# Kernel tuning notes

Measured on AMD Instinct MI355X. Metric: run time of the kernel, lower is better.

## Reference

```python
import jax, jax.numpy as jnp
import numpy as np

# Static config (matches init_kwargs)
T_Q, H_Q, W_Q = 8, 16, 16
T_K, H_K, W_K = 8, 16, 16
HEADS, QDIM = 8, 64


def _rel_dist(q_len, k_len):
    q_ratio = round(max(k_len / q_len, 1.0))
    k_ratio = round(max(q_len / k_len, 1.0))
    d = jnp.arange(q_len)[:, None] * q_ratio - jnp.arange(k_len)[None, :] * k_ratio
    return d + (k_len - 1) * k_ratio  # [q_len, k_len] int indices


def setup_inputs() -> dict:
    key = jax.random.key(0)
    k1, k2, k3, k4, k5 = jax.random.split(key, 5)
    B = 2
    q_tok = T_Q * H_Q * W_Q
    k_tok = T_K * H_K * W_K
    return {
        "query": jax.random.normal(k1, (B, HEADS, q_tok, QDIM), dtype=jnp.float32),
        "scores": jax.random.normal(k2, (B, HEADS, q_tok, k_tok), dtype=jnp.float32),
        "height_emb": jax.random.normal(k3, (2 * (max(H_Q, H_K) - 1) + 1, QDIM), dtype=jnp.float32),
        "width_emb": jax.random.normal(k4, (2 * (max(W_Q, W_K) - 1) + 1, QDIM), dtype=jnp.float32),
        "time_emb": jax.random.normal(k5, (2 * (max(T_Q, T_K) - 1) + 1, QDIM), dtype=jnp.float32),
    }


def reference(query, scores, height_emb, width_emb, time_emb):
    B = query.shape[0]
    # Relative-distance index tables (static)
    dist_h = _rel_dist(H_Q, H_K)  # [H_Q, H_K]
    dist_w = _rel_dist(W_Q, W_K)  # [W_Q, W_K]
    dist_t = _rel_dist(T_Q, T_K)  # [T_Q, T_K]
    Rh = height_emb[dist_h]  # [H_Q, H_K, C]
    Rw = width_emb[dist_w]   # [W_Q, W_K, C]
    Rt = time_emb[dist_t]    # [T_Q, T_K, C]
    q = query.reshape(B, HEADS, T_Q, H_Q, W_Q, QDIM)
    rel_h = jnp.einsum('bNthwc,hkc->bNthwk', q, Rh)  # k = key height
    rel_w = jnp.einsum('bNthwc,wkc->bNthwk', q, Rw)  # k = key width
    rel_t = jnp.einsum('bNthwc,tkc->bNthwk', q, Rt)  # k = key time
    s = scores.reshape(B, HEADS, T_Q, H_Q, W_Q, T_K, H_K, W_K)
    s = (s
         + rel_h[:, :, :, :, :, None, :, None]
         + rel_w[:, :, :, :, :, None, None, :]
         + rel_t[:, :, :, :, :, :, None, None])
    return s.reshape(B, HEADS, T_Q * H_Q * W_Q, T_K * H_K * W_K)
```

## Files before the change

kernel.cpp:

```cpp
#include <hip/hip_runtime.h>

#define T_Q 8
#define H_Q 16
#define W_Q 16
#define HEADS 8
#define QDIM 64
#define QTOK (T_Q * H_Q * W_Q)
#define KTOK 2048

__global__ __launch_bounds__(256)
void relpos_fused_kernel(const float* __restrict__ query,
                         const float* __restrict__ scores,
                         const float* __restrict__ hemb,
                         const float* __restrict__ wemb,
                         const float* __restrict__ temb,
                         float* __restrict__ out)
{
    const int row  = blockIdx.x;
    const int qtok = row & (QTOK - 1);
    const int t = (qtok >> 8) & 7;
    const int h = (qtok >> 4) & 15;
    const int w = qtok & 15;
    const int tid = threadIdx.x;

    __shared__ float q_s[QDIM];
    __shared__ float rel[40];

    if (tid < QDIM) q_s[tid] = query[(size_t)row * QDIM + tid];
    __syncthreads();

    if (tid < 40) {
        const float* emb;
        if (tid < 16) {
            emb = hemb + (size_t)(h - tid + 15) * QDIM;
        } else if (tid < 32) {
            emb = wemb + (size_t)(w - (tid - 16) + 15) * QDIM;
        } else {
            emb = temb + (size_t)(t - (tid - 32) + 7) * QDIM;
        }
        float acc = 0.f;
        #pragma unroll
        for (int c = 0; c < QDIM; c += 4) {
            float4 e = *reinterpret_cast<const float4*>(emb + c);
            acc += q_s[c]   * e.x;
            acc += q_s[c+1] * e.y;
            acc += q_s[c+2] * e.z;
            acc += q_s[c+3] * e.w;
        }
        rel[tid] = acc;
    }
    __syncthreads();

    const size_t base = (size_t)row * KTOK;
    #pragma unroll
    for (int it = 0; it < 2; ++it) {
        const int k4 = (it * 256 + tid) * 4;
        const int tk = k4 >> 8;
        const int hk = (k4 >> 4) & 15;
        const int wk = k4 & 15;
        const float add = rel[32 + tk] + rel[hk];
        float4 s = *reinterpret_cast<const float4*>(scores + base + k4);
        float4 o;
        o.x = s.x + add + rel[16 + wk + 0];
        o.y = s.y + add + rel[16 + wk + 1];
        o.z = s.z + add + rel[16 + wk + 2];
        o.w = s.w + add + rel[16 + wk + 3];
        *reinterpret_cast<float4*>(out + base + k4) = o;
    }
}

extern "C" void kernel_launch(void* const* d_in, const int* in_sizes, int n_in,
                              void* d_out, int out_size, void* d_ws, size_t ws_size,
                              hipStream_t stream) {
    const float* query  = (const float*)d_in[0];
    const float* scores = (const float*)d_in[1];
    const float* hemb   = (const float*)d_in[2];
    const float* wemb   = (const float*)d_in[3];
    const float* temb   = (const float*)d_in[4];
    float* out = (float*)d_out;

    const int B = in_sizes[0] / (HEADS * QTOK * QDIM);
    const int rows = B * HEADS * QTOK;

    relpos_fused_kernel<<<rows, 256, 0, stream>>>(query, scores, hemb, wemb, temb, out);
}
```

Measured before the change: 104.5 us.

## Map one wavefront per row and stream scores with nontemporal loads/stores

Each 256-thread block now handles four rows, one per 64-lane wavefront, so the grid shrinks by four. Every wave computes its own 40 relative-position dot products. Each lane keeps a fixed key h/w position across eight iterations, so the per-element adds are hoisted into registers. Scores and outputs use nontemporal loads and stores to skip cache pollution on this streaming, memory-bound workload, and the embedding dot product now reads q from shared memory as float4.

Result: faster. 100.5 us (-3.9%).

```diff
diff --git a/kernel.cpp b/kernel.cpp
--- a/kernel.cpp
+++ b/kernel.cpp
@@ -8,6 +8,8 @@
 #define QTOK (T_Q * H_Q * W_Q)
 #define KTOK 2048
 
+typedef float f32x4 __attribute__((ext_vector_type(4)));
+
 __global__ __launch_bounds__(256)
 void relpos_fused_kernel(const float* __restrict__ query,
                          const float* __restrict__ scores,
@@ -16,56 +18,63 @@
                          const float* __restrict__ temb,
                          float* __restrict__ out)
 {
-    const int row  = blockIdx.x;
+    const int tid  = threadIdx.x;
+    const int wid  = tid >> 6;
+    const int lane = tid & 63;
+    const int row  = blockIdx.x * 4 + wid;
     const int qtok = row & (QTOK - 1);
     const int t = (qtok >> 8) & 7;
     const int h = (qtok >> 4) & 15;
     const int w = qtok & 15;
-    const int tid = threadIdx.x;
 
-    __shared__ float q_s[QDIM];
-    __shared__ float rel[40];
+    __shared__ float q_s[4][QDIM];
+    __shared__ float rel[4][40];
 
-    if (tid < QDIM) q_s[tid] = query[(size_t)row * QDIM + tid];
+    q_s[wid][lane] = __builtin_nontemporal_load(query + (size_t)row * QDIM + lane);
     __syncthreads();
 
-    if (tid < 40) {
+    if (lane < 40) {
         const float* emb;
-        if (tid < 16) {
-            emb = hemb + (size_t)(h - tid + 15) * QDIM;
-        } else if (tid < 32) {
-            emb = wemb + (size_t)(w - (tid - 16) + 15) * QDIM;
+        if (lane < 16) {
+            emb = hemb + (size_t)(h - lane + 15) * QDIM;
+        } else if (lane < 32) {
+            emb = wemb + (size_t)(w - (lane - 16) + 15) * QDIM;
         } else {
-            emb = temb + (size_t)(t - (tid - 32) + 7) * QDIM;
+            emb = temb + (size_t)(t - (lane - 32) + 7) * QDIM;
         }
         float acc = 0.f;
         #pragma unroll
         for (int c = 0; c < QDIM; c += 4) {
-            float4 e = *reinterpret_cast<const float4*>(emb + c);
-            acc += q_s[c]   * e.x;
-            acc += q_s[c+1] * e.y;
-            acc += q_s[c+2] * e.z;
-            acc += q_s[c+3] * e.w;
+            f32x4 e  = *reinterpret_cast<const f32x4*>(emb + c);
+            f32x4 qv = *reinterpret_cast<const f32x4*>(&q_s[wid][c]);
+            acc += qv.x * e.x + qv.y * e.y + qv.z * e.z + qv.w * e.w;
         }
-        rel[tid] = acc;
+        rel[wid][lane] = acc;
     }
     __syncthreads();
 
-    const size_t base = (size_t)row * KTOK;
+    const float rh  = rel[wid][lane >> 2];
+    const int   wk0 = (lane & 3) * 4;
+    const float add0 = rh + rel[wid][16 + wk0 + 0];
+    const float add1 = rh + rel[wid][16 + wk0 + 1];
+    const float add2 = rh + rel[wid][16 + wk0 + 2];
+    const float add3 = rh + rel[wid][16 + wk0 + 3];
+    float rt[8];
     #pragma unroll
-    for (int it = 0; it < 2; ++it) {
-        const int k4 = (it * 256 + tid) * 4;
-        const int tk = k4 >> 8;
-        const int hk = (k4 >> 4) & 15;
-        const int wk = k4 & 15;
-        const float add = rel[32 + tk] + rel[hk];
-        float4 s = *reinterpret_cast<const float4*>(scores + base + k4);
-        float4 o;
-        o.x = s.x + add + rel[16 + wk + 0];
-        o.y = s.y + add + rel[16 + wk + 1];
-        o.z = s.z + add + rel[16 + wk + 2];
-        o.w = s.w + add + rel[16 + wk + 3];
-        *reinterpret_cast<float4*>(out + base + k4) = o;
+    for (int it = 0; it < 8; ++it) rt[it] = rel[wid][32 + it];
+
+    const size_t base = (size_t)row * KTOK + lane * 4;
+    #pragma unroll
+    for (int it = 0; it < 8; ++it) {
+        const f32x4 s = __builtin_nontemporal_load(
+            reinterpret_cast<const f32x4*>(scores + base + it * 256));
+        f32x4 o;
+        o.x = s.x + add0 + rt[it];
+        o.y = s.y + add1 + rt[it];
+        o.z = s.z + add2 + rt[it];
+        o.w = s.w + add3 + rt[it];
+        __builtin_nontemporal_store(o,
+            reinterpret_cast<f32x4*>(out + base + it * 256));
     }
 }
 
@@ -82,5 +91,5 @@
     const int B = in_sizes[0] / (HEADS * QTOK * QDIM);
     const int rows = B * HEADS * QTOK;
 
-    relpos_fused_kernel<<<rows, 256, 0, stream>>>(query, scores, hemb, wemb, temb, out);
+    relpos_fused_kernel<<<rows / 4, 256, 0, stream>>>(query, scores, hemb, wemb, temb, out);
 }
```
